# Performance work log

Measured on AMD Instinct MI355X. Metric: run time of the kernel, lower is better.

Reference implementation:

```python
import jax, jax.numpy as jnp
import numpy as np

Q, A, R, S, K = 256, 28, 512, 256, 2  # n_quantize, n_aux, n_resch, n_skipch, kernel_size
DEPTH, REPEAT = 10, 3
L = DEPTH * REPEAT  # 30 layers
T = 8192


def setup_inputs() -> dict:
    key = jax.random.key(0)
    ks = jax.random.split(key, 24)
    w = lambda k, shape: jax.random.normal(k, shape, dtype=jnp.float32) * 0.05
    return {
        "x": jax.random.randint(ks[0], (1, T), 0, Q, dtype=jnp.int32),
        "h": jax.random.normal(ks[1], (1, A, T), dtype=jnp.float32),
        "Wc": w(ks[2], (R, Q, K)), "bc": w(ks[3], (R,)),
        "Wds": w(ks[4], (L, R, R, K)), "bds": w(ks[5], (L, R)),
        "Wdt": w(ks[6], (L, R, R, K)), "bdt": w(ks[7], (L, R)),
        "Was": w(ks[8], (L, R, A, 1)), "bas": w(ks[9], (L, R)),
        "Wat": w(ks[10], (L, R, A, 1)), "bat": w(ks[11], (L, R)),
        "Wsk": w(ks[12], (L, S, R, 1)), "bsk": w(ks[13], (L, S)),
        "Wr": w(ks[14], (L, R, R, 1)), "br": w(ks[15], (L, R)),
        "Wp1": w(ks[16], (S, S, 1)), "bp1": w(ks[17], (S,)),
        "Wp2": w(ks[18], (Q, S, 1)), "bp2": w(ks[19], (Q,)),
    }


def _cconv(z, w, b, d):
    # causal dilated conv: z [1,C,T], w [O,C,K] -> [1,O,T]
    pad = (w.shape[2] - 1) * d
    y = jax.lax.conv_general_dilated(
        z, w, window_strides=(1,), padding=[(pad, 0)], rhs_dilation=(d,),
        dimension_numbers=("NCH", "OIH", "NCH"))
    return y + b[None, :, None]


def reference(x, h, Wc, bc, Wds, bds, Wdt, bdt, Was, bas, Wat, bat,
              Wsk, bsk, Wr, br, Wp1, bp1, Wp2, bp2):
    dilations = [2 ** i for i in range(DEPTH)] * REPEAT
    oh = jax.nn.one_hot(x, Q, dtype=Wc.dtype).transpose(0, 2, 1)  # [1,Q,T]
    out = _cconv(oh, Wc, bc, 1)  # [1,R,T]
    skip_sum = jnp.zeros((1, S, oh.shape[2]), dtype=Wc.dtype)
    for l, d in enumerate(dilations):
        s = _cconv(out, Wds[l], bds[l], d) + _cconv(h, Was[l], bas[l], 1)
        t = _cconv(out, Wdt[l], bdt[l], d) + _cconv(h, Wat[l], bat[l], 1)
        g = jax.nn.sigmoid(s) * jnp.tanh(t)  # gated activation
        skip_sum = skip_sum + _cconv(g, Wsk[l], bsk[l], 1)
        out = _cconv(g, Wr[l], br[l], 1) + out  # residual
    o = jax.nn.relu(skip_sum)
    o = jax.nn.relu(_cconv(o, Wp1, bp1, 1))
    o = _cconv(o, Wp2, bp2, 1)  # [1,Q,T]
    return o[0].T  # [T,Q], matches squeeze(0).transpose(0,1)
```

## Files before the change

### kernel.cpp

```cpp
#include <hip/hip_runtime.h>
#include <hip/hip_bf16.h>
#include <math.h>
#include <stdint.h>

#define T_LEN 8192
#define RCH   512
#define SCH   256
#define QCH   256
#define ACH   28
#define NLAYER 30
#define KGATE 1088
#define KSR   512
#define KPOST 256

typedef _Float16 f16x8 __attribute__((ext_vector_type(8)));
typedef float    f32x4 __attribute__((ext_vector_type(4)));

static __device__ __forceinline__ unsigned short f2h(float v) {
    _Float16 h = (_Float16)v;
    return *reinterpret_cast<unsigned short*>(&h);
}

#define G2L(SRC, DST) __builtin_amdgcn_global_load_lds(                        \
    (__attribute__((address_space(1))) void*)(const void*)(SRC),              \
    (__attribute__((address_space(3))) void*)(void*)(DST), 16, 0, 0)

__global__ void pack_gate_v(const float* __restrict__ Wds,
                            const float* __restrict__ Wdt,
                            const float* __restrict__ Was,
                            const float* __restrict__ Wat,
                            unsigned short* __restrict__ dst) {
    int l = blockIdx.y;
    int c = blockIdx.x * 256 + threadIdx.x;
    int tile = c >> 6, lane = c & 63;
    int mt = tile / 34, kt = tile % 34;
    int m  = mt * 16 + (lane & 15);
    int k0 = kt * 32 + (lane >> 4) * 8;
    int br = m & 1, ch = m >> 1;
    const float* Wd = (br ? Wdt : Wds) + (size_t)l * RCH * RCH * 2;
    const float* Wa = (br ? Wat : Was) + (size_t)l * RCH * ACH;
    unsigned short o[8];
    if (k0 < 512) {
        const float* base = Wd + ((size_t)ch * 512 + k0) * 2;
        #pragma unroll
        for (int q = 0; q < 4; ++q) {
            float4 v = *(const float4*)(base + q * 4);
            o[q * 2 + 0] = f2h(v.x);
            o[q * 2 + 1] = f2h(v.z);
        }
    } else if (k0 < 1024) {
        const float* base = Wd + ((size_t)ch * 512 + (k0 - 512)) * 2;
        #pragma unroll
        for (int q = 0; q < 4; ++q) {
            float4 v = *(const float4*)(base + q * 4);
            o[q * 2 + 0] = f2h(v.y);
            o[q * 2 + 1] = f2h(v.w);
        }
    } else {
        int a0 = k0 - 1024;
        #pragma unroll
        for (int i = 0; i < 8; ++i)
            o[i] = (a0 + i < ACH) ? f2h(Wa[(size_t)ch * ACH + a0 + i]) : (unsigned short)0;
    }
    *(uint4*)&dst[(size_t)l * 1024 * KGATE + (size_t)tile * 512 + lane * 8] = *(uint4*)o;
}

__global__ void pack_sr_v(const float* __restrict__ Wsk,
                          const float* __restrict__ Wr,
                          unsigned short* __restrict__ dst) {
    int l = blockIdx.y;
    int c = blockIdx.x * 256 + threadIdx.x;
    int tile = c >> 6, lane = c & 63;
    int mt = tile >> 4, kt = tile & 15;
    int m  = mt * 16 + (lane & 15);
    int k0 = kt * 32 + (lane >> 4) * 8;
    const float* row = (m < SCH) ? (Wsk + (size_t)l * SCH * RCH + (size_t)m * 512)
                                 : (Wr  + (size_t)l * RCH * RCH + (size_t)(m - SCH) * 512);
    float4 v0 = *(const float4*)(row + k0);
    float4 v1 = *(const float4*)(row + k0 + 4);
    unsigned short o[8] = { f2h(v0.x), f2h(v0.y), f2h(v0.z), f2h(v0.w),
                            f2h(v1.x), f2h(v1.y), f2h(v1.z), f2h(v1.w) };
    *(uint4*)&dst[(size_t)l * 768 * KSR + (size_t)tile * 512 + lane * 8] = *(uint4*)o;
}

__global__ void pack_post_v(const float* __restrict__ W,
                            unsigned short* __restrict__ dst) {
    int c = blockIdx.x * 256 + threadIdx.x;
    int tile = c >> 6, lane = c & 63;
    int mt = tile >> 3, kt = tile & 7;
    int m  = mt * 16 + (lane & 15);
    int k0 = kt * 32 + (lane >> 4) * 8;
    float4 v0 = *(const float4*)(W + (size_t)m * 256 + k0);
    float4 v1 = *(const float4*)(W + (size_t)m * 256 + k0 + 4);
    unsigned short o[8] = { f2h(v0.x), f2h(v0.y), f2h(v0.z), f2h(v0.w),
                            f2h(v1.x), f2h(v1.y), f2h(v1.z), f2h(v1.w) };
    *(uint4*)&dst[(size_t)tile * 512 + lane * 8] = *(uint4*)o;
}

__global__ void transpose_wc(const float* __restrict__ Wc,
                             float* __restrict__ WcT) {
    int idx = blockIdx.x * 256 + threadIdx.x;
    int r = idx >> 9;
    int qt = idx & 511;
    int q = qt >> 1, tap = qt & 1;
    WcT[(size_t)q * 1024 + tap * 512 + r] = Wc[(size_t)r * 512 + qt];
}

__global__ void embed_v(const int* __restrict__ x,
                        const float* __restrict__ WcT,
                        const float* __restrict__ bc,
                        float* __restrict__ out_tm,
                        unsigned short* __restrict__ outhf) {
    int idx = blockIdx.x * 256 + threadIdx.x;
    int t = idx >> 6, rc = (idx & 63) * 8;
    int x1 = x[t];
    const float* w1 = WcT + (size_t)x1 * 1024 + 512 + rc;
    float4 a = *(const float4*)w1;
    float4 b = *(const float4*)(w1 + 4);
    float4 c0 = *(const float4*)(bc + rc);
    float4 c1 = *(const float4*)(bc + rc + 4);
    a.x += c0.x; a.y += c0.y; a.z += c0.z; a.w += c0.w;
    b.x += c1.x; b.y += c1.y; b.z += c1.z; b.w += c1.w;
    if (t > 0) {
        const float* w0 = WcT + (size_t)x[t - 1] * 1024 + rc;
        float4 d0 = *(const float4*)w0;
        float4 d1 = *(const float4*)(w0 + 4);
        a.x += d0.x; a.y += d0.y; a.z += d0.z; a.w += d0.w;
        b.x += d1.x; b.y += d1.y; b.z += d1.z; b.w += d1.w;
    }
    size_t o = (size_t)t * 512 + rc;
    *(float4*)&out_tm[o] = a;
    *(float4*)&out_tm[o + 4] = b;
    unsigned short p[8] = { f2h(a.x), f2h(a.y), f2h(a.z), f2h(a.w),
                            f2h(b.x), f2h(b.y), f2h(b.z), f2h(b.w) };
    *(uint4*)&outhf[o + 512 * 512] = *(uint4*)p;
}

__global__ void packh_kernel(const float* __restrict__ h,
                             unsigned short* __restrict__ h_tm) {
    int idx = blockIdx.x * 256 + threadIdx.x;
    int t = idx >> 6, a = idx & 63;
    h_tm[idx] = f2h(a < ACH ? h[(size_t)a * T_LEN + t] : 0.f);
}

__global__ void reluconv_v(const float* __restrict__ skip,
                           unsigned short* __restrict__ dst) {
    int idx = (blockIdx.x * 256 + threadIdx.x) * 8;
    float4 v0 = *(const float4*)(skip + idx);
    float4 v1 = *(const float4*)(skip + idx + 4);
    unsigned short o[8] = { f2h(fmaxf(v0.x, 0.f)), f2h(fmaxf(v0.y, 0.f)),
                            f2h(fmaxf(v0.z, 0.f)), f2h(fmaxf(v0.w, 0.f)),
                            f2h(fmaxf(v1.x, 0.f)), f2h(fmaxf(v1.y, 0.f)),
                            f2h(fmaxf(v1.z, 0.f)), f2h(fmaxf(v1.w, 0.f)) };
    *(uint4*)&dst[idx] = *(uint4*)o;
}

template<int MODE, int KT64, int MB>
__global__ __launch_bounds__(256) void mfma_gemm(
    const unsigned short* __restrict__ Apk,
    const unsigned short* __restrict__ B0,
    const unsigned short* __restrict__ B2,
    const float* __restrict__ bias0, const float* __restrict__ bias1,
    const float* __restrict__ bias2, const float* __restrict__ bias3,
    float* __restrict__ O0, float* __restrict__ O1,
    unsigned short* __restrict__ OB, int dil)
{
    constexpr int KT32 = KT64 * 2;
    constexpr int NWG = MB * 64;
    constexpr int CPX = NWG / 8;

    __shared__ unsigned short Bsm[2][128 * 64];

    const int tid  = threadIdx.x;
    const int lane = tid & 63, wave = tid >> 6;
    const int wm = wave & 1, wn = wave >> 1;

    const int bid = blockIdx.x;
    const int swz = (bid & 7) * CPX + (bid >> 3);
    const int mb  = swz % MB;
    const int tb  = swz / MB;
    const int m0  = mb * 128;
    const int t0  = tb * 128;

    const int kc   = ((lane & 7) ^ (lane >> 3)) * 8;
    const int rsub = lane >> 3;

    auto stage_tile = [&](int kt, int buf) {
        const int kb = kt * 64;
        #pragma unroll
        for (int j = 0; j < 4; ++j) {
            const int row = wave * 32 + j * 8 + rsub;
            const int tg  = t0 + row;
            const unsigned short* src;
            if constexpr (MODE == 0) {
                if (kb < 512)
                    src = B0 + (size_t)(512 + tg - dil) * 512 + kb + kc;
                else if (kb < 1024)
                    src = B0 + (size_t)(512 + tg) * 512 + (kb - 512) + kc;
                else
                    src = B2 + (size_t)tg * 64 + kc;
            } else if constexpr (MODE == 1) {
                src = B0 + (size_t)tg * 512 + kb + kc;
            } else {
                src = B0 + (size_t)tg * 256 + kb + kc;
            }
            G2L(src, &Bsm[buf][(wave * 4 + j) * 512]);
        }
    };

    f32x4 acc[4][4];
    #pragma unroll
    for (int a = 0; a < 4; ++a)
        #pragma unroll
        for (int b = 0; b < 4; ++b) acc[a][b] = (f32x4){0.f, 0.f, 0.f, 0.f};

    const size_t mt0 = (size_t)(mb * 8) + wm * 4;

    stage_tile(0, 0);
    __syncthreads();

    int cur = 0;
    for (int kt = 0; kt < KT64; ++kt, cur ^= 1) {
        if (kt + 1 < KT64) stage_tile(kt + 1, cur ^ 1);

        f16x8 afr[4][2];
        #pragma unroll
        for (int mi = 0; mi < 4; ++mi)
            #pragma unroll
            for (int ks = 0; ks < 2; ++ks)
                afr[mi][ks] = *(const f16x8*)(Apk +
                    ((mt0 + mi) * KT32 + (size_t)(kt * 2 + ks)) * 512 + lane * 8);

        f16x8 bfr[4][2];
        #pragma unroll
        for (int ni = 0; ni < 4; ++ni)
            #pragma unroll
            for (int ks = 0; ks < 2; ++ks) {
                const int trow = wn * 64 + ni * 16 + (lane & 15);
                const int kch  = ks * 4 + (lane >> 4);
                const int sch  = kch ^ (lane & 7);
                bfr[ni][ks] = *(const f16x8*)&Bsm[cur][trow * 64 + sch * 8];
            }

        #pragma unroll
        for (int mi = 0; mi < 4; ++mi)
            #pragma unroll
            for (int ni = 0; ni < 4; ++ni) {
                acc[mi][ni] = __builtin_amdgcn_mfma_f32_16x16x32_f16(
                    afr[mi][0], bfr[ni][0], acc[mi][ni], 0, 0, 0);
                acc[mi][ni] = __builtin_amdgcn_mfma_f32_16x16x32_f16(
                    afr[mi][1], bfr[ni][1], acc[mi][ni], 0, 0, 0);
            }

        __syncthreads();
    }

    const int rb0 = (lane >> 4) * 4;
    #pragma unroll
    for (int mi = 0; mi < 4; ++mi) {
        #pragma unroll
        for (int ni = 0; ni < 4; ++ni) {
            int m = m0 + wm * 64 + mi * 16 + rb0;
            int t = t0 + wn * 64 + ni * 16 + (lane & 15);
            f32x4 v = acc[mi][ni];
            if constexpr (MODE == 0) {
                int c0 = m >> 1;
                float s0 = v.x + bias0[c0]     + bias2[c0];
                float tv0 = v.y + bias1[c0]     + bias3[c0];
                float s1 = v.z + bias0[c0 + 1] + bias2[c0 + 1];
                float tv1 = v.w + bias1[c0 + 1] + bias3[c0 + 1];
                float g0 = (1.f / (1.f + __expf(-s0))) * tanhf(tv0);
                float g1 = (1.f / (1.f + __expf(-s1))) * tanhf(tv1);
                unsigned int p = (unsigned int)f2h(g0) | ((unsigned int)f2h(g1) << 16);
                *(unsigned int*)&OB[(size_t)t * 512 + c0] = p;
            } else if constexpr (MODE == 1) {
                if (m < SCH) {
                    float4* p = (float4*)&O0[(size_t)t * 256 + m];
                    float4 o = *p;
                    o.x += v.x + bias0[m + 0];
                    o.y += v.y + bias0[m + 1];
                    o.z += v.z + bias0[m + 2];
                    o.w += v.w + bias0[m + 3];
                    *p = o;
                } else {
                    int c = m - SCH;
                    float4* p = (float4*)&O1[(size_t)t * 512 + c];
                    float4 o = *p;
                    o.x += v.x + bias1[c + 0];
                    o.y += v.y + bias1[c + 1];
                    o.z += v.z + bias1[c + 2];
                    o.w += v.w + bias1[c + 3];
                    *p = o;
                    uint2 pk;
                    pk.x = (unsigned int)f2h(o.x) | ((unsigned int)f2h(o.y) << 16);
                    pk.y = (unsigned int)f2h(o.z) | ((unsigned int)f2h(o.w) << 16);
                    *(uint2*)&OB[(size_t)(512 + t) * 512 + c] = pk;
                }
            } else if constexpr (MODE == 2) {
                float o0 = fmaxf(v.x + bias0[m + 0], 0.f);
                float o1 = fmaxf(v.y + bias0[m + 1], 0.f);
                float o2 = fmaxf(v.z + bias0[m + 2], 0.f);
                float o3 = fmaxf(v.w + bias0[m + 3], 0.f);
                uint2 pk;
                pk.x = (unsigned int)f2h(o0) | ((unsigned int)f2h(o1) << 16);
                pk.y = (unsigned int)f2h(o2) | ((unsigned int)f2h(o3) << 16);
                *(uint2*)&OB[(size_t)t * 256 + m] = pk;
            } else {
                float4 o;
                o.x = v.x + bias0[m + 0];
                o.y = v.y + bias0[m + 1];
                o.z = v.z + bias0[m + 2];
                o.w = v.w + bias0[m + 3];
                *(float4*)&O0[(size_t)t * 256 + m] = o;
            }
        }
    }
}

extern "C" void kernel_launch(void* const* d_in, const int* in_sizes, int n_in,
                              void* d_out, int out_size, void* d_ws, size_t ws_size,
                              hipStream_t stream) {
    const int*   x   = (const int*)  d_in[0];
    const float* h   = (const float*)d_in[1];
    const float* Wc  = (const float*)d_in[2];
    const float* bc  = (const float*)d_in[3];
    const float* Wds = (const float*)d_in[4];
    const float* bds = (const float*)d_in[5];
    const float* Wdt = (const float*)d_in[6];
    const float* bdt = (const float*)d_in[7];
    const float* Was = (const float*)d_in[8];
    const float* bas = (const float*)d_in[9];
    const float* Wat = (const float*)d_in[10];
    const float* bat = (const float*)d_in[11];
    const float* Wsk = (const float*)d_in[12];
    const float* bsk = (const float*)d_in[13];
    const float* Wr  = (const float*)d_in[14];
    const float* br  = (const float*)d_in[15];
    const float* Wp1 = (const float*)d_in[16];
    const float* bp1 = (const float*)d_in[17];
    const float* Wp2 = (const float*)d_in[18];
    const float* bp2 = (const float*)d_in[19];
    float* dout = (float*)d_out;

    const size_t WG_EL  = (size_t)1024 * KGATE;
    const size_t WSR_EL = (size_t)768 * KSR;
    char* w = (char*)d_ws;
    float*          out_tm = (float*)w;               w += (size_t)T_LEN * 512 * 4;
    unsigned short* outhf  = (unsigned short*)w;      w += (size_t)(T_LEN + 512) * 512 * 2;
    unsigned short* g_tm   = (unsigned short*)w;      w += (size_t)T_LEN * 512 * 2;
    unsigned short* h_tm   = (unsigned short*)w;      w += (size_t)T_LEN * 64 * 2;
    unsigned short* skiphf = (unsigned short*)w;      w += (size_t)T_LEN * 256 * 2;
    unsigned short* o1hf   = (unsigned short*)w;      w += (size_t)T_LEN * 256 * 2;
    unsigned short* Wp1_pk = (unsigned short*)w;      w += (size_t)256 * 256 * 2;
    unsigned short* Wp2_pk = (unsigned short*)w;      w += (size_t)256 * 256 * 2;
    float*          WcT    = (float*)w;               w += (size_t)QCH * 2 * RCH * 4;
    unsigned short* Wg_pk  = (unsigned short*)w;
    size_t used_base = (size_t)((char*)Wg_pk - (char*)d_ws);
    size_t need_bulk = used_base + (WG_EL + WSR_EL) * NLAYER * 2;
    const bool bulk = ws_size >= need_bulk;
    unsigned short* Wsr_pk = Wg_pk + (bulk ? WG_EL * NLAYER : WG_EL);
    float* skip = dout;

    hipMemsetAsync(skip, 0, (size_t)T_LEN * 256 * 4, stream);
    hipMemsetAsync(outhf, 0, (size_t)512 * 512 * 2, stream);

    transpose_wc<<<1024, 256, 0, stream>>>(Wc, WcT);
    embed_v<<<(T_LEN * 64) / 256, 256, 0, stream>>>(x, WcT, bc, out_tm, outhf);
    packh_kernel<<<(T_LEN * 64) / 256, 256, 0, stream>>>(h, h_tm);
    pack_post_v<<<32, 256, 0, stream>>>(Wp1, Wp1_pk);
    pack_post_v<<<32, 256, 0, stream>>>(Wp2, Wp2_pk);

    if (bulk) {
        pack_gate_v<<<dim3(544, NLAYER), 256, 0, stream>>>(Wds, Wdt, Was, Wat, Wg_pk);
        pack_sr_v<<<dim3(192, NLAYER), 256, 0, stream>>>(Wsk, Wr, Wsr_pk);
    }

    for (int l = 0; l < NLAYER; ++l) {
        int dil = 1 << (l % 10);
        const unsigned short* wg;
        const unsigned short* wsr;
        if (bulk) {
            wg  = Wg_pk  + (size_t)l * WG_EL;
            wsr = Wsr_pk + (size_t)l * WSR_EL;
        } else {
            pack_gate_v<<<dim3(544, 1), 256, 0, stream>>>(
                Wds + (size_t)l * RCH * RCH * 2, Wdt + (size_t)l * RCH * RCH * 2,
                Was + (size_t)l * RCH * ACH, Wat + (size_t)l * RCH * ACH, Wg_pk);
            pack_sr_v<<<dim3(192, 1), 256, 0, stream>>>(
                Wsk + (size_t)l * SCH * RCH, Wr + (size_t)l * RCH * RCH, Wsr_pk);
            wg = Wg_pk; wsr = Wsr_pk;
        }
        mfma_gemm<0, KGATE / 64, 8><<<512, 256, 0, stream>>>(
            wg, outhf, h_tm,
            bds + (size_t)l * RCH, bdt + (size_t)l * RCH,
            bas + (size_t)l * RCH, bat + (size_t)l * RCH,
            nullptr, nullptr, g_tm, dil);
        mfma_gemm<1, KSR / 64, 6><<<384, 256, 0, stream>>>(
            wsr, g_tm, nullptr,
            bsk + (size_t)l * SCH, br + (size_t)l * RCH, nullptr, nullptr,
            skip, out_tm, outhf, 0);
    }

    reluconv_v<<<(T_LEN * 256 / 8) / 256, 256, 0, stream>>>(skip, skiphf);
    mfma_gemm<2, KPOST / 64, 2><<<128, 256, 0, stream>>>(
        Wp1_pk, skiphf, nullptr, bp1, nullptr, nullptr, nullptr,
        nullptr, nullptr, o1hf, 0);
    mfma_gemm<3, KPOST / 64, 2><<<128, 256, 0, stream>>>(
        Wp2_pk, o1hf, nullptr, bp2, nullptr, nullptr, nullptr,
        dout, nullptr, nullptr, 0);
}
```

Baseline: 1.764 ms.

## Double-buffer A fragments, use manual waitcnt barriers, and use fast sigmoid/tanh

Restructures the GEMM main loop so the next tile's global-to-LDS stage and the next A-fragment global loads are issued before the current tile's MFMAs. Two A register buffers alternate between iterations. The full __syncthreads is replaced with explicit s_waitcnt on vmcnt/lgkmcnt plus s_barrier, with sched_barriers pinning the instruction order. The gate epilogue now uses an rcp-based sigmoid and computes tanh as 2*sigmoid(2x)-1. This costs extra registers, relies on a hand-counted vmcnt that must match the number of outstanding loads, and may give slightly different rounding than tanhf.

```diff
diff --git a/kernel.cpp b/kernel.cpp
--- a/kernel.cpp
+++ b/kernel.cpp
@@ -16,9 +16,15 @@
 typedef _Float16 f16x8 __attribute__((ext_vector_type(8)));
 typedef float    f32x4 __attribute__((ext_vector_type(4)));
 
+#define SB0() __builtin_amdgcn_sched_barrier(0)
+
 static __device__ __forceinline__ unsigned short f2h(float v) {
     _Float16 h = (_Float16)v;
     return *reinterpret_cast<unsigned short*>(&h);
+}
+
+static __device__ __forceinline__ float fsig(float x) {
+    return __builtin_amdgcn_rcpf(1.f + __expf(-x));
 }
 
 #define G2L(SRC, DST) __builtin_amdgcn_global_load_lds(                        \
@@ -185,6 +191,16 @@
     const int kc   = ((lane & 7) ^ (lane >> 3)) * 8;
     const int rsub = lane >> 3;
 
+    const size_t mt0 = (size_t)(mb * 8) + wm * 4;
+
+    f32x4 acc[4][4];
+    #pragma unroll
+    for (int a = 0; a < 4; ++a)
+        #pragma unroll
+        for (int b = 0; b < 4; ++b) acc[a][b] = (f32x4){0.f, 0.f, 0.f, 0.f};
+
+    f16x8 afrA[4][2], afrB[4][2], bfr[4][2];
+
     auto stage_tile = [&](int kt, int buf) {
         const int kb = kt * 64;
         #pragma unroll
@@ -208,30 +224,16 @@
         }
     };
 
-    f32x4 acc[4][4];
-    #pragma unroll
-    for (int a = 0; a < 4; ++a)
-        #pragma unroll
-        for (int b = 0; b < 4; ++b) acc[a][b] = (f32x4){0.f, 0.f, 0.f, 0.f};
-
-    const size_t mt0 = (size_t)(mb * 8) + wm * 4;
-
-    stage_tile(0, 0);
-    __syncthreads();
-
-    int cur = 0;
-    for (int kt = 0; kt < KT64; ++kt, cur ^= 1) {
-        if (kt + 1 < KT64) stage_tile(kt + 1, cur ^ 1);
-
-        f16x8 afr[4][2];
+    auto load_afr = [&](int kt, f16x8 (&dst)[4][2]) {
         #pragma unroll
         for (int mi = 0; mi < 4; ++mi)
             #pragma unroll
             for (int ks = 0; ks < 2; ++ks)
-                afr[mi][ks] = *(const f16x8*)(Apk +
+                dst[mi][ks] = *(const f16x8*)(Apk +
                     ((mt0 + mi) * KT32 + (size_t)(kt * 2 + ks)) * 512 + lane * 8);
-
-        f16x8 bfr[4][2];
+    };
+
+    auto load_bfr = [&](int buf) {
         #pragma unroll
         for (int ni = 0; ni < 4; ++ni)
             #pragma unroll
@@ -239,20 +241,49 @@
                 const int trow = wn * 64 + ni * 16 + (lane & 15);
                 const int kch  = ks * 4 + (lane >> 4);
                 const int sch  = kch ^ (lane & 7);
-                bfr[ni][ks] = *(const f16x8*)&Bsm[cur][trow * 64 + sch * 8];
+                bfr[ni][ks] = *(const f16x8*)&Bsm[buf][trow * 64 + sch * 8];
             }
-
+    };
+
+    auto do_mfma = [&](f16x8 (&A)[4][2]) {
         #pragma unroll
         for (int mi = 0; mi < 4; ++mi)
             #pragma unroll
             for (int ni = 0; ni < 4; ++ni) {
                 acc[mi][ni] = __builtin_amdgcn_mfma_f32_16x16x32_f16(
-                    afr[mi][0], bfr[ni][0], acc[mi][ni], 0, 0, 0);
+                    A[mi][0], bfr[ni][0], acc[mi][ni], 0, 0, 0);
                 acc[mi][ni] = __builtin_amdgcn_mfma_f32_16x16x32_f16(
-                    afr[mi][1], bfr[ni][1], acc[mi][ni], 0, 0, 0);
+                    A[mi][1], bfr[ni][1], acc[mi][ni], 0, 0, 0);
             }
-
-        __syncthreads();
+    };
+
+    stage_tile(0, 0);
+    SB0();
+    load_afr(0, afrA);
+    SB0();
+    asm volatile("s_waitcnt vmcnt(8)" ::: "memory");
+    SB0();
+    __builtin_amdgcn_s_barrier();
+
+    #pragma unroll
+    for (int kt = 0; kt < KT64; ++kt) {
+        const int cur = kt & 1;
+        if (kt + 1 < KT64) {
+            stage_tile(kt + 1, cur ^ 1);
+            SB0();
+            if (cur) load_afr(kt + 1, afrA);
+            else     load_afr(kt + 1, afrB);
+            SB0();
+        }
+        load_bfr(cur);
+        if (cur) do_mfma(afrB);
+        else     do_mfma(afrA);
+        if (kt + 1 < KT64) {
+            SB0();
+            asm volatile("s_waitcnt vmcnt(8) lgkmcnt(0)" ::: "memory");
+            SB0();
+            __builtin_amdgcn_s_barrier();
+        }
     }
 
     const int rb0 = (lane >> 4) * 4;
@@ -269,8 +300,8 @@
                 float tv0 = v.y + bias1[c0]     + bias3[c0];
                 float s1 = v.z + bias0[c0 + 1] + bias2[c0 + 1];
                 float tv1 = v.w + bias1[c0 + 1] + bias3[c0 + 1];
-                float g0 = (1.f / (1.f + __expf(-s0))) * tanhf(tv0);
-                float g1 = (1.f / (1.f + __expf(-s1))) * tanhf(tv1);
+                float g0 = fsig(s0) * (2.f * fsig(2.f * tv0) - 1.f);
+                float g1 = fsig(s1) * (2.f * fsig(2.f * tv1) - 1.f);
                 unsigned int p = (unsigned int)f2h(g0) | ((unsigned int)f2h(g1) << 16);
                 *(unsigned int*)&OB[(size_t)t * 512 + c0] = p;
             } else if constexpr (MODE == 1) {
```

New measurement: 1.545 ms. 12.4% less time.
